# Optimization experiments

Hardware: AMD Instinct MI355X
Metric: run time of the kernel (lower is better)

The kernel has to match this reference:

```python
import jax, jax.numpy as jnp
import numpy as np
from jax import lax

B, N, D, L, EDGE_H, NGNN = 8, 128, 256, 64, 64, 3


def setup_inputs() -> dict:
    key = jax.random.key(0)
    ks = iter(jax.random.split(key, 64))
    def nrm(shape, s=0.02):
        return jax.random.normal(next(ks), shape, jnp.float32) * s
    inp = {}
    inp["node_feats"] = jax.random.uniform(next(ks), (B, N, 11), jnp.float32)
    inp["edge_feats"] = jax.random.normal(next(ks), (B, N, N, 3), jnp.float32)
    inp["adj_mask"] = jax.random.randint(next(ks), (B, N, N), 0, 2).astype(bool)
    inp["layer_costs"] = jax.random.uniform(next(ks), (B, L), jnp.float32)
    inp["global_dynamic"] = jax.random.uniform(next(ks), (B, 2), jnp.float32)
    inp["p_node_w"] = nrm((11, D)); inp["p_node_b"] = jnp.zeros((D,), jnp.float32)
    inp["g_w1"] = nrm((NGNN, D + 3, EDGE_H)); inp["g_b1"] = jnp.zeros((NGNN, EDGE_H), jnp.float32)
    inp["g_w2"] = nrm((NGNN, EDGE_H, D)); inp["g_b2"] = jnp.zeros((NGNN, D), jnp.float32)
    inp["u_w1"] = nrm((NGNN, 3 * D, D)); inp["u_b1"] = jnp.zeros((NGNN, D), jnp.float32)
    inp["u_w2"] = nrm((NGNN, D, D)); inp["u_b2"] = jnp.zeros((NGNN, D), jnp.float32)
    inp["ln_g"] = jnp.ones((NGNN, D), jnp.float32); inp["ln_b"] = jnp.zeros((NGNN, D), jnp.float32)
    inp["conv_w"] = nrm((32, 1, 4)); inp["conv_b"] = jnp.zeros((32,), jnp.float32)
    inp["lp_w"] = nrm((32 * 31, D)); inp["lp_b"] = jnp.zeros((D,), jnp.float32)
    inp["q_w"] = nrm((2 * D + 2, D)); inp["q_b"] = jnp.zeros((D,), jnp.float32)
    inp["k_w"] = nrm((D, D)); inp["k_b"] = jnp.zeros((D,), jnp.float32)
    inp["s_w1"] = nrm((D + 2, D)); inp["s_b1"] = jnp.zeros((D,), jnp.float32)
    inp["s_w2"] = nrm((D, 1)); inp["s_b2"] = jnp.zeros((1,), jnp.float32)
    inp["v_w1"] = nrm((2 * D + 2, D)); inp["v_b1"] = jnp.zeros((D,), jnp.float32)
    inp["v_w2"] = nrm((D, 1)); inp["v_b2"] = jnp.zeros((1,), jnp.float32)
    return inp


def _ecgc(h, edge_feats, adj_bool, gw1, gb1, gw2, gb2, uw1, ub1, uw2, ub2, lng, lnb):
    Bh, Nn, Dd = h.shape
    # h_j: features of sender node j broadcast over receiver axis -> (B, N, N, D)
    h_j = jnp.broadcast_to(h[:, None, :, :], (Bh, Nn, Nn, Dd))
    gate_in = jnp.concatenate([h_j, edge_feats], axis=-1)            # (B,N,N,D+3)
    gates = jax.nn.sigmoid(jax.nn.relu(gate_in @ gw1 + gb1) @ gw2 + gb2)
    msg = gates * h_j                                                # (B,N,N,D)
    m = adj_bool.astype(h.dtype)[..., None]
    cnt = jnp.maximum(m.sum(axis=2), 1.0)                            # (B,N,1)
    agg_mean = (msg * m).sum(axis=2) / cnt                           # (B,N,D)
    agg_max = jnp.where(adj_bool[..., None], msg, -jnp.inf).max(axis=2)
    agg_max = jnp.where(jnp.isinf(agg_max), 0.0, agg_max)
    ui = jnp.concatenate([h, agg_mean, agg_max], axis=-1)            # (B,N,3D)
    x = h + (jax.nn.relu(ui @ uw1 + ub1) @ uw2 + ub2)
    mu = x.mean(-1, keepdims=True)
    var = ((x - mu) ** 2).mean(-1, keepdims=True)
    return (x - mu) * lax.rsqrt(var + 1e-5) * lng + lnb


def reference(node_feats, edge_feats, adj_mask, layer_costs, global_dynamic,
              p_node_w, p_node_b, g_w1, g_b1, g_w2, g_b2, u_w1, u_b1, u_w2, u_b2,
              ln_g, ln_b, conv_w, conv_b, lp_w, lp_b, q_w, q_b, k_w, k_b,
              s_w1, s_b1, s_w2, s_b2, v_w1, v_b1, v_w2, v_b2):
    # layer cost encoder: Conv1d(1,32,k=4,s=2) + ReLU, flatten, Linear
    le = lax.conv_general_dilated(layer_costs[:, None, :], conv_w, (2,), 'VALID',
                                  dimension_numbers=('NCH', 'OIH', 'NCH'))
    le = jax.nn.relu(le + conv_b[None, :, None])                     # (B,32,31)
    layer_embed = le.reshape(le.shape[0], -1) @ lp_w + lp_b          # (B,D)
    h = node_feats @ p_node_w + p_node_b                             # (B,N,D)
    for i in range(g_w1.shape[0]):
        h = _ecgc(h, edge_feats, adj_mask, g_w1[i], g_b1[i], g_w2[i], g_b2[i],
                  u_w1[i], u_b1[i], u_w2[i], u_b2[i], ln_g[i], ln_b[i])
    w = (node_feats[:, :, 0] * node_feats[:, :, 7])[..., None]       # (B,N,1)
    graph_embed = (w * h).sum(axis=1) / jnp.maximum(w.sum(axis=1), 1e-8)
    qi = jnp.concatenate([graph_embed, layer_embed, global_dynamic], axis=-1)
    query = qi @ q_w + q_b                                           # (B,D)
    keys = h @ k_w + k_b                                             # (B,N,D)
    device_scores = jnp.einsum('bnd,bd->bn', keys, query) / jnp.sqrt(jnp.float32(query.shape[-1]))
    si = jnp.concatenate([graph_embed, global_dynamic], axis=-1)
    stop_logit = jax.nn.relu(si @ s_w1 + s_b1) @ s_w2 + s_b2         # (B,1)
    all_logits = jnp.concatenate([device_scores, stop_logit], axis=1)
    value = jax.nn.relu(qi @ v_w1 + v_b1) @ v_w2 + v_b2              # (B,1)
    return all_logits, value, h
```

## Files before the change

kernel.cpp:

```cpp
#include <hip/hip_runtime.h>
#include <hip/hip_bf16.h>
#include <math.h>

#define BB 8
#define NN_ 128
#define DD 256
#define LL 64
#define EH 64
#define NG 3

typedef __attribute__((ext_vector_type(8))) short bs8;
typedef __attribute__((ext_vector_type(4))) float f4;

__device__ __forceinline__ short f2bf(float f) {
    __hip_bfloat16 h = __float2bfloat16(f);
    return *reinterpret_cast<short*>(&h);
}

__device__ __forceinline__ float blockReduceSum(float v, float* sRed) {
    int tid = threadIdx.x;
    __syncthreads();
    sRed[tid] = v;
    __syncthreads();
    for (int s = 128; s > 0; s >>= 1) {
        if (tid < s) sRed[tid] += sRed[tid + s];
        __syncthreads();
    }
    return sRed[0];
}

__global__ __launch_bounds__(256) void k_detect(const unsigned char* __restrict__ adj,
                                                int* __restrict__ mode) {
    __shared__ int sOff, sBig;
    const int tid = threadIdx.x;
    if (tid == 0) { sOff = 0; sBig = 0; }
    __syncthreads();
    int off = 0, big = 0;
    #pragma unroll
    for (int k = 0; k < 4; ++k) {
        unsigned char v = adj[tid * 4 + k];
        if (v > 1) big = 1;
        if (k != 0 && v != 0) off = 1;
    }
    if (off) atomicOr(&sOff, 1);
    if (big) atomicOr(&sBig, 1);
    __syncthreads();
    if (tid == 0) mode[0] = sBig ? 2 : (sOff ? 0 : 1);
}

__global__ __launch_bounds__(256) void k_prep(
    const float* __restrict__ uw1, const float* __restrict__ uw2,
    unsigned short* __restrict__ w1t, unsigned short* __restrict__ w2t)
{
    const int blk = blockIdx.x, tid = threadIdx.x;
    const float* src; unsigned short* dst; int K, kt, dt;
    if (blk < 144) {
        int l = blk / 48, t = blk % 48; kt = t >> 2; dt = t & 3;
        src = uw1 + (size_t)l * 768 * 256; dst = w1t + (size_t)l * 256 * 768; K = 768;
    } else {
        int x = blk - 144; int l = x / 16, t = x % 16; kt = t >> 2; dt = t & 3;
        src = uw2 + (size_t)l * 65536; dst = w2t + (size_t)l * 65536; K = 256;
    }
    __shared__ float sT[64][65];
    #pragma unroll
    for (int q = 0; q < 16; ++q) {
        int idx = q * 256 + tid;
        int kk = idx >> 6, dd = idx & 63;
        sT[kk][dd] = src[(size_t)(kt * 64 + kk) * 256 + dt * 64 + dd];
    }
    __syncthreads();
    const int d = tid >> 2, kc = (tid & 3) * 16;
    unsigned short* drow = dst + (size_t)(dt * 64 + d) * K + kt * 64 + kc;
    #pragma unroll
    for (int i = 0; i < 16; ++i) drow[i] = (unsigned short)f2bf(sT[kc + i][d]);
}

__global__ __launch_bounds__(256) void k_prepg(
    const float* __restrict__ gw2, unsigned short* __restrict__ g2t)
{
    const int blk = blockIdx.x, tid = threadIdx.x;
    const int l = blk >> 2, dt = blk & 3;
    const float* src = gw2 + (size_t)l * 64 * 256;
    unsigned short* dst = g2t + (size_t)l * 256 * 64;
    __shared__ float sT[64][65];
    #pragma unroll
    for (int q = 0; q < 16; ++q) {
        int idx = q * 256 + tid;
        int kk = idx >> 6, dd = idx & 63;
        sT[kk][dd] = src[(size_t)kk * 256 + dt * 64 + dd];
    }
    __syncthreads();
    const int d = tid >> 2, kc = (tid & 3) * 16;
    unsigned short* drow = dst + (size_t)(dt * 64 + d) * 64 + kc;
    #pragma unroll
    for (int i = 0; i < 16; ++i) drow[i] = (unsigned short)f2bf(sT[kc + i][d]);
}

__global__ __launch_bounds__(256) void k_nodeproj(
    const float* __restrict__ nf, const float* __restrict__ w,
    const float* __restrict__ bias, float* __restrict__ h)
{
    const int row = blockIdx.x, tid = threadIdx.x;
    __shared__ float sF[11];
    if (tid < 11) sF[tid] = nf[(size_t)row * 11 + tid];
    __syncthreads();
    float a = bias[tid];
    #pragma unroll
    for (int f = 0; f < 11; ++f) a += sF[f] * w[f * DD + tid];
    h[(size_t)row * DD + tid] = a;
}

__global__ __launch_bounds__(256) void k_conv(
    const float* __restrict__ lc, const float* __restrict__ cw,
    const float* __restrict__ cb, float* __restrict__ conv)
{
    const int b = blockIdx.x, tid = threadIdx.x;
    __shared__ float sC[LL];
    if (tid < LL) sC[tid] = lc[b * LL + tid];
    __syncthreads();
    for (int idx = tid; idx < 992; idx += 256) {
        int c = idx / 31, t = idx % 31;
        float a = cb[c];
        #pragma unroll
        for (int k = 0; k < 4; ++k) a += sC[2 * t + k] * cw[c * 4 + k];
        conv[b * 992 + idx] = fmaxf(a, 0.f);
    }
}

__global__ __launch_bounds__(256) void k_lmm(
    const float* __restrict__ conv, const float* __restrict__ lpw,
    float* __restrict__ part)
{
    const int blk = blockIdx.x;
    const int b = blk >> 5, kseg = (blk >> 2) & 7, c4 = blk & 3;
    const int tid = threadIdx.x;
    const int d = tid & 63, ss = tid >> 6;
    __shared__ float sV[124];
    __shared__ float sP[4][64];
    if (tid < 124) sV[tid] = conv[b * 992 + kseg * 124 + tid];
    __syncthreads();
    float acc = 0.f;
    for (int k = ss; k < 124; k += 4)
        acc += sV[k] * lpw[(size_t)(kseg * 124 + k) * DD + c4 * 64 + d];
    sP[ss][d] = acc;
    __syncthreads();
    if (ss == 0)
        part[(b * 32 + kseg * 4 + c4) * 64 + d] = sP[0][d] + sP[1][d] + sP[2][d] + sP[3][d];
}

__global__ __launch_bounds__(256) void k_lred(
    const float* __restrict__ part, const float* __restrict__ lpb,
    float* __restrict__ le)
{
    const int b = blockIdx.x, tid = threadIdx.x;
    const int c4 = tid >> 6, d = tid & 63;
    float a = lpb[tid];
    #pragma unroll
    for (int kseg = 0; kseg < 8; ++kseg)
        a += part[(b * 32 + kseg * 4 + c4) * 64 + d];
    le[b * DD + tid] = a;
}

__global__ __launch_bounds__(256) void k_pregate(
    const float* __restrict__ h, const float* __restrict__ gw1,
    const float* __restrict__ gb1, float* __restrict__ preg)
{
    const int tid = threadIdx.x;
    const int row0 = blockIdx.x * 4;
    const int r = tid >> 6, t = tid & 63;
    __shared__ float sH[4][DD];
    for (int idx = tid; idx < 4 * DD; idx += 256)
        sH[idx >> 8][idx & 255] = h[(size_t)row0 * DD + idx];
    __syncthreads();
    float a = gb1[t];
    for (int k = 0; k < DD; ++k) a += sH[r][k] * gw1[k * EH + t];
    preg[(size_t)(row0 + r) * EH + t] = a;
}

template<int PRE>
__global__ __launch_bounds__(256) void k_edge(
    const float* __restrict__ h, const float* __restrict__ preg,
    const float* __restrict__ edge, const void* __restrict__ adj,
    const int* __restrict__ mode,
    const float* __restrict__ gw1,
    const float* __restrict__ gw2,
    const unsigned short* __restrict__ g2t,
    const float* __restrict__ gb2,
    float* __restrict__ agg_mean, float* __restrict__ agg_max)
{
    const int tid = threadIdx.x;
    const int bi = blockIdx.x;
    const int b = bi >> 7;
    const int lane = tid & 63, w = tid >> 6;
    const int lrow = lane >> 4, lcol = lane & 15;
    const int md = mode[0];

    __shared__ __align__(16) unsigned int sHid[4096];
    __shared__ __align__(16) unsigned short sB[PRE ? 16 : 16384];
    __shared__ float sWe[192];
    __shared__ float sE[384];
    __shared__ unsigned long long sMask[2];

    if (tid < 192) sWe[tid] = gw1[16384 + tid];
    const float* eB = edge + (size_t)bi * 384;
    for (int idx = tid; idx < 384; idx += 256) sE[idx] = eB[idx];
    if (tid < 128) {
        int mv;
        if (md == 1)      mv = ((const int*)adj)[(size_t)bi * NN_ + tid] != 0;
        else if (md == 2) mv = ((const float*)adj)[(size_t)bi * NN_ + tid] != 0.f;
        else              mv = ((const unsigned char*)adj)[(size_t)bi * NN_ + tid] != 0;
        unsigned long long bal = __ballot(mv);
        if ((tid & 63) == 0) sMask[tid >> 6] = bal;
    }
    __syncthreads();

    const float* pB = preg + (size_t)b * NN_ * EH;
    #pragma unroll
    for (int q = 0; q < 16; ++q) {
        int idx = q * 256 + tid;
        int j = idx >> 5, p = idx & 31;
        float2 pv = *(const float2*)(pB + j * EH + 2 * p);
        float e0 = sE[j * 3], e1 = sE[j * 3 + 1], e2 = sE[j * 3 + 2];
        int t0 = 2 * p, t1 = t0 + 1;
        float v0 = fmaxf(pv.x + e0 * sWe[t0] + e1 * sWe[64 + t0] + e2 * sWe[128 + t0], 0.f);
        float v1 = fmaxf(pv.y + e0 * sWe[t1] + e1 * sWe[64 + t1] + e2 * sWe[128 + t1], 0.f);
        unsigned int pk = (unsigned int)(unsigned short)f2bf(v0) |
                          ((unsigned int)(unsigned short)f2bf(v1) << 16);
        sHid[j * 32 + (p ^ ((j & 7) << 2))] = pk;
    }
    if constexpr (!PRE) {
        #pragma unroll
        for (int q = 0; q < 64; ++q) {
            int idx = q * 256 + tid;
            int k = idx >> 8, d = idx & 255;
            sB[(d * 64 + k) ^ ((d & 7) << 3)] = (unsigned short)f2bf(gw2[idx]);
        }
    }
    __syncthreads();

    const unsigned long long m0 = sMask[0], m1 = sMask[1];
    const float cntf = (float)(__popcll(m0) + __popcll(m1));

    bs8 bfr[4][2];
    float bg[4];
    #pragma unroll
    for (int nt = 0; nt < 4; ++nt) {
        int d = w * 64 + nt * 16 + lcol;
        bg[nt] = gb2[d];
        #pragma unroll
        for (int ks = 0; ks < 2; ++ks) {
            int k0 = ks * 32 + lrow * 8;
            if constexpr (PRE)
                bfr[nt][ks] = *(const bs8*)(g2t + (size_t)d * 64 + k0);
            else
                bfr[nt][ks] = *(const bs8*)(sB + ((d * 64 + k0) ^ ((d & 7) << 3)));
        }
    }

    const float* hB = h + (size_t)b * NN_ * DD;
    float vs[4] = {0.f, 0.f, 0.f, 0.f};
    float vm[4] = {-INFINITY, -INFINITY, -INFINITY, -INFINITY};

    #pragma unroll
    for (int pp = 0; pp < 2; ++pp) {
        f4 acc[4][4] = {};
        #pragma unroll
        for (int ks = 0; ks < 2; ++ks) {
            bs8 afr[4];
            #pragma unroll
            for (int m = 0; m < 4; ++m) {
                int j = pp * 64 + m * 16 + lcol;
                int k0 = ks * 32 + lrow * 8;
                afr[m] = *(const bs8*)(sHid + (j * 32 + ((k0 >> 1) ^ ((j & 7) << 2))));
            }
            #pragma unroll
            for (int m = 0; m < 4; ++m)
                #pragma unroll
                for (int nt = 0; nt < 4; ++nt)
                    acc[m][nt] = __builtin_amdgcn_mfma_f32_16x16x32_bf16(
                        afr[m], bfr[nt][ks], acc[m][nt], 0, 0, 0);
        }
        const unsigned long long mw = pp ? m1 : m0;
        #pragma unroll
        for (int m = 0; m < 4; ++m) {
            #pragma unroll
            for (int nt = 0; nt < 4; ++nt) {
                int dnt = w * 64 + nt * 16 + lcol;
                #pragma unroll
                for (int r = 0; r < 4; ++r) {
                    int bit = m * 16 + lrow * 4 + r;
                    float x = acc[m][nt][r] + bg[nt];
                    float g = __builtin_amdgcn_rcpf(1.0f + __expf(-x));
                    float msg = g * hB[(pp * 64 + bit) * DD + dnt];
                    int on = (int)((mw >> bit) & 1ULL);
                    vs[nt] += on ? msg : 0.f;
                    vm[nt] = fmaxf(vm[nt], on ? msg : -INFINITY);
                }
            }
        }
    }

    #pragma unroll
    for (int nt = 0; nt < 4; ++nt) {
        float s = vs[nt];
        s += __shfl_xor(s, 16); s += __shfl_xor(s, 32);
        vs[nt] = s;
        float m = vm[nt];
        m = fmaxf(m, __shfl_xor(m, 16)); m = fmaxf(m, __shfl_xor(m, 32));
        vm[nt] = m;
    }
    const int g = lrow;
    float ssel = (g == 0) ? vs[0] : (g == 1) ? vs[1] : (g == 2) ? vs[2] : vs[3];
    float msel = (g == 0) ? vm[0] : (g == 1) ? vm[1] : (g == 2) ? vm[2] : vm[3];
    const int d = w * 64 + lane;
    agg_mean[(size_t)bi * DD + d] = ssel / fmaxf(cntf, 1.f);
    agg_max[(size_t)bi * DD + d] = (cntf > 0.f) ? msel : 0.f;
}

__global__ __launch_bounds__(256) void k_upd(
    const float* __restrict__ h, const float* __restrict__ amean,
    const float* __restrict__ amax,
    const unsigned short* __restrict__ w1t,
    const float* __restrict__ ub1,
    const unsigned short* __restrict__ w2t,
    const float* __restrict__ ub2,
    const float* __restrict__ lng, const float* __restrict__ lnb,
    float* __restrict__ hout, float* __restrict__ out2)
{
    const int tid = threadIdx.x;
    const int row0 = blockIdx.x * 4;
    const int lane = tid & 63, w = tid >> 6;
    const int lcol = lane & 15, lrow = lane >> 4;

    __shared__ __align__(16) unsigned int sX32[16 * 384];
    __shared__ __align__(16) unsigned short sH16[16 * 256];
    __shared__ float sRes[4][256];
    __shared__ float sOut[4][256];

    {
        const int j = w;
        const float* hR = h + (size_t)(row0 + j) * DD;
        const float* mR = amean + (size_t)(row0 + j) * DD;
        const float* xR = amax + (size_t)(row0 + j) * DD;
        #pragma unroll
        for (int q = 0; q < 6; ++q) {
            int p = lane + q * 64;
            int k = 2 * p;
            float2 v;
            if (k < 256)      { v = *(const float2*)(hR + k); sRes[j][k] = v.x; sRes[j][k + 1] = v.y; }
            else if (k < 512)   v = *(const float2*)(mR + (k - 256));
            else                v = *(const float2*)(xR + (k - 512));
            unsigned int pk = (unsigned int)(unsigned short)f2bf(v.x) |
                              ((unsigned int)(unsigned short)f2bf(v.y) << 16);
            sX32[j * 384 + (p ^ (j << 2))] = pk;
        }
    }
    __syncthreads();

    const char* sXb = (const char*)sX32;
    const unsigned short* w1r = w1t + (size_t)(w * 64 + lcol) * 768;
    f4 a0 = {0.f, 0.f, 0.f, 0.f}, a1 = a0, a2 = a0, a3 = a0;
    #pragma unroll 4
    for (int ks = 0; ks < 24; ++ks) {
        int k0 = ks * 32 + lrow * 8;
        bs8 av = *(const bs8*)(sXb + lcol * 1536 + ((((k0 >> 3) ^ (lcol & 7))) << 4));
        bs8 b0 = *(const bs8*)(w1r + k0);
        bs8 b1 = *(const bs8*)(w1r + 16 * 768 + k0);
        bs8 b2 = *(const bs8*)(w1r + 32 * 768 + k0);
        bs8 b3 = *(const bs8*)(w1r + 48 * 768 + k0);
        a0 = __builtin_amdgcn_mfma_f32_16x16x32_bf16(av, b0, a0, 0, 0, 0);
        a1 = __builtin_amdgcn_mfma_f32_16x16x32_bf16(av, b1, a1, 0, 0, 0);
        a2 = __builtin_amdgcn_mfma_f32_16x16x32_bf16(av, b2, a2, 0, 0, 0);
        a3 = __builtin_amdgcn_mfma_f32_16x16x32_bf16(av, b3, a3, 0, 0, 0);
    }
    if (lrow == 0) {
        #pragma unroll
        for (int nt = 0; nt < 4; ++nt) {
            int d = w * 64 + nt * 16 + lcol;
            float bb = ub1[d];
            f4 A = (nt == 0) ? a0 : (nt == 1) ? a1 : (nt == 2) ? a2 : a3;
            #pragma unroll
            for (int r = 0; r < 4; ++r) {
                float hv = fmaxf(A[r] + bb, 0.f);
                sH16[r * 256 + (d ^ (r << 3))] = (unsigned short)f2bf(hv);
            }
        }
    }
    __syncthreads();

    const unsigned short* w2r = w2t + (size_t)(w * 64 + lcol) * 256;
    f4 c0 = {0.f, 0.f, 0.f, 0.f}, c1 = c0, c2 = c0, c3 = c0;
    #pragma unroll
    for (int ks = 0; ks < 8; ++ks) {
        int k0 = ks * 32 + lrow * 8;
        bs8 av = *(const bs8*)((const char*)sH16 + lcol * 512 + ((((k0 >> 3) ^ (lcol & 7))) << 4));
        bs8 b0 = *(const bs8*)(w2r + k0);
        bs8 b1 = *(const bs8*)(w2r + 16 * 256 + k0);
        bs8 b2 = *(const bs8*)(w2r + 32 * 256 + k0);
        bs8 b3 = *(const bs8*)(w2r + 48 * 256 + k0);
        c0 = __builtin_amdgcn_mfma_f32_16x16x32_bf16(av, b0, c0, 0, 0, 0);
        c1 = __builtin_amdgcn_mfma_f32_16x16x32_bf16(av, b1, c1, 0, 0, 0);
        c2 = __builtin_amdgcn_mfma_f32_16x16x32_bf16(av, b2, c2, 0, 0, 0);
        c3 = __builtin_amdgcn_mfma_f32_16x16x32_bf16(av, b3, c3, 0, 0, 0);
    }
    if (lrow == 0) {
        #pragma unroll
        for (int nt = 0; nt < 4; ++nt) {
            int d = w * 64 + nt * 16 + lcol;
            float bb = ub2[d];
            f4 C = (nt == 0) ? c0 : (nt == 1) ? c1 : (nt == 2) ? c2 : c3;
            #pragma unroll
            for (int r = 0; r < 4; ++r)
                sOut[r][d] = C[r] + bb + sRes[r][d];
        }
    }
    __syncthreads();

    float xv[4], s = 0.f;
    #pragma unroll
    for (int q = 0; q < 4; ++q) { xv[q] = sOut[w][lane + 64 * q]; s += xv[q]; }
    #pragma unroll
    for (int off = 1; off < 64; off <<= 1) s += __shfl_xor(s, off);
    const float mu = s * (1.f / DD);
    float s2 = 0.f;
    #pragma unroll
    for (int q = 0; q < 4; ++q) { float d = xv[q] - mu; s2 += d * d; }
    #pragma unroll
    for (int off = 1; off < 64; off <<= 1) s2 += __shfl_xor(s2, off);
    const float inv = rsqrtf(s2 * (1.f / DD) + 1e-5f);
    #pragma unroll
    for (int q = 0; q < 4; ++q) {
        int c = lane + 64 * q;
        float res = (xv[q] - mu) * inv * lng[c] + lnb[c];
        hout[(size_t)(row0 + w) * DD + c] = res;
        if (out2) out2[(size_t)(row0 + w) * DD + c] = res;
    }
}

__global__ __launch_bounds__(256) void k_update(
    const float* __restrict__ agg_mean, const float* __restrict__ agg_max,
    const float* __restrict__ uw1, const float* __restrict__ ub1,
    const float* __restrict__ uw2, const float* __restrict__ ub2,
    const float* __restrict__ lng, const float* __restrict__ lnb,
    float* __restrict__ h, float* __restrict__ out2)
{
    const int tid = threadIdx.x;
    const int row0 = blockIdx.x * 4;
    __shared__ float sUi[4][3 * DD];
    __shared__ float sHid[4][DD];
    __shared__ float sRed[256];
    for (int idx = tid; idx < 4 * 3 * DD; idx += 256) {
        int r = idx / (3 * DD), k = idx % (3 * DD);
        int row = row0 + r;
        float v;
        if (k < DD)            v = h[(size_t)row * DD + k];
        else if (k < 2 * DD)   v = agg_mean[(size_t)row * DD + (k - DD)];
        else                   v = agg_max[(size_t)row * DD + (k - 2 * DD)];
        sUi[r][k] = v;
    }
    __syncthreads();
    float b1 = ub1[tid];
    float a0 = b1, a1 = b1, a2 = b1, a3 = b1;
    for (int k = 0; k < 3 * DD; ++k) {
        float wv = uw1[k * DD + tid];
        a0 += sUi[0][k] * wv; a1 += sUi[1][k] * wv;
        a2 += sUi[2][k] * wv; a3 += sUi[3][k] * wv;
    }
    sHid[0][tid] = fmaxf(a0, 0.f); sHid[1][tid] = fmaxf(a1, 0.f);
    sHid[2][tid] = fmaxf(a2, 0.f); sHid[3][tid] = fmaxf(a3, 0.f);
    __syncthreads();
    float b2 = ub2[tid];
    float x[4] = {b2, b2, b2, b2};
    for (int k = 0; k < DD; ++k) {
        float wv = uw2[k * DD + tid];
        x[0] += sHid[0][k] * wv; x[1] += sHid[1][k] * wv;
        x[2] += sHid[2][k] * wv; x[3] += sHid[3][k] * wv;
    }
    #pragma unroll
    for (int r = 0; r < 4; ++r) x[r] += h[(size_t)(row0 + r) * DD + tid];
    const float g = lng[tid], be = lnb[tid];
    for (int r = 0; r < 4; ++r) {
        float mu = blockReduceSum(x[r], sRed) * (1.f / DD);
        float dc = x[r] - mu;
        float var = blockReduceSum(dc * dc, sRed) * (1.f / DD);
        float res = dc * rsqrtf(var + 1e-5f) * g + be;
        h[(size_t)(row0 + r) * DD + tid] = res;
        if (out2) out2[(size_t)(row0 + r) * DD + tid] = res;
    }
}

__global__ __launch_bounds__(256) void k_gembed(
    const float* __restrict__ nf, const float* __restrict__ h, float* __restrict__ ge)
{
    const int b = blockIdx.x, tid = threadIdx.x;
    __shared__ float sW[NN_];
    __shared__ float sRed[256];
    if (tid < NN_) {
        const float* p = nf + ((size_t)b * NN_ + tid) * 11;
        sW[tid] = p[0] * p[7];
    }
    __syncthreads();
    float part = (tid < NN_) ? sW[tid] : 0.f;
    float wsum = blockReduceSum(part, sRed);
    float acc = 0.f;
    for (int n = 0; n < NN_; ++n) acc += sW[n] * h[((size_t)b * NN_ + n) * DD + tid];
    ge[b * DD + tid] = acc / fmaxf(wsum, 1e-8f);
}

__global__ __launch_bounds__(256) void k_hmm(
    const float* __restrict__ ge, const float* __restrict__ le,
    const float* __restrict__ gd,
    const float* __restrict__ qw, const float* __restrict__ sw1,
    const float* __restrict__ vw1, float* __restrict__ part)
{
    const int blk = blockIdx.x;
    const int m = blk >> 5, kseg = (blk >> 2) & 7, c4 = blk & 3;
    const int tid = threadIdx.x;
    const int d = tid & 63, ks = tid >> 6;
    const int K = (m == 1) ? 258 : 514;
    const int kc = (m == 1) ? 33 : 65;
    const int k0 = kseg * kc;
    const int klen = min(k0 + kc, K) - k0;
    __shared__ float sX[8 * 66];
    __shared__ float sP[4][8][64];
    for (int idx = tid; idx < 8 * kc; idx += 256) {
        int b = idx / kc, kk = idx % kc, k = k0 + kk;
        float v = 0.f;
        if (k < K) {
            if (m == 1) v = (k < 256) ? ge[b * DD + k] : gd[b * 2 + (k - 256)];
            else        v = (k < 256) ? ge[b * DD + k]
                          : (k < 512) ? le[b * DD + (k - 256)]
                                      : gd[b * 2 + (k - 512)];
        }
        sX[b * 66 + kk] = v;
    }
    __syncthreads();
    const float* W = (m == 0) ? qw : (m == 1) ? sw1 : vw1;
    const int dg = c4 * 64 + d;
    float acc[8] = {0.f, 0.f, 0.f, 0.f, 0.f, 0.f, 0.f, 0.f};
    for (int kk = ks; kk < klen; kk += 4) {
        float wv = W[(size_t)(k0 + kk) * DD + dg];
        #pragma unroll
        for (int b = 0; b < 8; ++b) acc[b] += sX[b * 66 + kk] * wv;
    }
    #pragma unroll
    for (int b = 0; b < 8; ++b) sP[ks][b][d] = acc[b];
    __syncthreads();
    for (int idx = tid; idx < 8 * 64; idx += 256) {
        int b = idx >> 6, dd = idx & 63;
        float sum = sP[0][b][dd] + sP[1][b][dd] + sP[2][b][dd] + sP[3][b][dd];
        part[((m * 8 + kseg) * 8 + b) * DD + c4 * 64 + dd] = sum;
    }
}

__global__ __launch_bounds__(256) void k_hfin(
    const float* __restrict__ part,
    const float* __restrict__ qb, const float* __restrict__ sb1,
    const float* __restrict__ vb1,
    const float* __restrict__ sw2, const float* __restrict__ sb2,
    const float* __restrict__ vw2, const float* __restrict__ vb2,
    float* __restrict__ query, float* __restrict__ out)
{
    const int b = blockIdx.x, tid = threadIdx.x;
    __shared__ float sRed[256];
    float q = qb[tid], s = sb1[tid], v = vb1[tid];
    #pragma unroll
    for (int kseg = 0; kseg < 8; ++kseg) {
        q += part[((0 * 8 + kseg) * 8 + b) * DD + tid];
        s += part[((1 * 8 + kseg) * 8 + b) * DD + tid];
        v += part[((2 * 8 + kseg) * 8 + b) * DD + tid];
    }
    query[b * DD + tid] = q;
    s = fmaxf(s, 0.f); v = fmaxf(v, 0.f);
    float stop = blockReduceSum(s * sw2[tid], sRed);
    float val  = blockReduceSum(v * vw2[tid], sRed);
    if (tid == 0) {
        out[b * 129 + 128] = stop + sb2[0];
        out[1032 + b] = val + vb2[0];
    }
}

__global__ __launch_bounds__(256) void k_scores(
    const float* __restrict__ h, const float* __restrict__ kw,
    const float* __restrict__ kb, const float* __restrict__ query,
    float* __restrict__ out)
{
    const int tid = threadIdx.x;
    const int row0 = blockIdx.x * 4;
    __shared__ float sH[4][DD];
    __shared__ float sRed[256];
    for (int idx = tid; idx < 4 * DD; idx += 256)
        sH[idx >> 8][idx & 255] = h[(size_t)row0 * DD + idx];
    __syncthreads();
    float bb = kb[tid];
    float a0 = bb, a1 = bb, a2 = bb, a3 = bb;
    for (int k = 0; k < DD; ++k) {
        float wv = kw[k * DD + tid];
        a0 += sH[0][k] * wv; a1 += sH[1][k] * wv;
        a2 += sH[2][k] * wv; a3 += sH[3][k] * wv;
    }
    const int b = row0 >> 7;
    const float q = query[b * DD + tid];
    float s0 = blockReduceSum(a0 * q, sRed);
    float s1 = blockReduceSum(a1 * q, sRed);
    float s2 = blockReduceSum(a2 * q, sRed);
    float s3 = blockReduceSum(a3 * q, sRed);
    if (tid == 0) {
        int n0 = row0 & (NN_ - 1);
        out[b * 129 + n0 + 0] = s0 * 0.0625f;
        out[b * 129 + n0 + 1] = s1 * 0.0625f;
        out[b * 129 + n0 + 2] = s2 * 0.0625f;
        out[b * 129 + n0 + 3] = s3 * 0.0625f;
    }
}

extern "C" void kernel_launch(void* const* d_in, const int* in_sizes, int n_in,
                              void* d_out, int out_size, void* d_ws, size_t ws_size,
                              hipStream_t stream) {
    (void)in_sizes; (void)n_in; (void)out_size;
    const float* nf  = (const float*)d_in[0];
    const float* ef  = (const float*)d_in[1];
    const void*  adj = d_in[2];
    const float* lc  = (const float*)d_in[3];
    const float* gd  = (const float*)d_in[4];
    const float* pnw = (const float*)d_in[5];
    const float* pnb = (const float*)d_in[6];
    const float* gw1 = (const float*)d_in[7];
    const float* gb1 = (const float*)d_in[8];
    const float* gw2 = (const float*)d_in[9];
    const float* gb2 = (const float*)d_in[10];
    const float* uw1 = (const float*)d_in[11];
    const float* ub1 = (const float*)d_in[12];
    const float* uw2 = (const float*)d_in[13];
    const float* ub2 = (const float*)d_in[14];
    const float* lng = (const float*)d_in[15];
    const float* lnb = (const float*)d_in[16];
    const float* cw  = (const float*)d_in[17];
    const float* cb  = (const float*)d_in[18];
    const float* lpw = (const float*)d_in[19];
    const float* lpb = (const float*)d_in[20];
    const float* qw  = (const float*)d_in[21];
    const float* qb  = (const float*)d_in[22];
    const float* kw  = (const float*)d_in[23];
    const float* kb  = (const float*)d_in[24];
    const float* sw1 = (const float*)d_in[25];
    const float* sb1 = (const float*)d_in[26];
    const float* sw2 = (const float*)d_in[27];
    const float* sb2 = (const float*)d_in[28];
    const float* vw1 = (const float*)d_in[29];
    const float* vb1 = (const float*)d_in[30];
    const float* vw2 = (const float*)d_in[31];
    const float* vb2 = (const float*)d_in[32];

    float* ws = (float*)d_ws;
    float* h     = ws;
    float* preg  = ws + 262144;
    float* amean = ws + 327680;
    float* amax  = ws + 589824;
    float* le    = ws + 851968;
    float* ge    = ws + 854016;
    float* query = ws + 856064;
    int*   mode  = (int*)(ws + 862208);
    unsigned short* uw1t = (unsigned short*)(ws + 862212);
    unsigned short* uw2t = (unsigned short*)(ws + 1157124);
    unsigned short* g2t  = (unsigned short*)(ws + 1255428);
    const size_t NEED = (size_t)1280004 * 4;
    const bool pre = ws_size >= NEED;
    float* conv  = amax;
    float* lpart = amean;
    float* hpart = amean;
    float* out   = (float*)d_out;

    k_detect<<<1, 256, 0, stream>>>((const unsigned char*)adj, mode);
    if (pre) {
        k_prep<<<192, 256, 0, stream>>>(uw1, uw2, uw1t, uw2t);
        k_prepg<<<12, 256, 0, stream>>>(gw2, g2t);
    }
    k_nodeproj<<<BB * NN_, 256, 0, stream>>>(nf, pnw, pnb, h);
    k_conv<<<BB, 256, 0, stream>>>(lc, cw, cb, conv);
    k_lmm<<<256, 256, 0, stream>>>(conv, lpw, lpart);
    k_lred<<<BB, 256, 0, stream>>>(lpart, lpb, le);
    for (int i = 0; i < NG; ++i) {
        const float* gw1i = gw1 + (size_t)i * 259 * EH;
        float* out2sel = (i == NG - 1) ? (out + 1040) : (float*)nullptr;
        k_pregate<<<BB * NN_ / 4, 256, 0, stream>>>(h, gw1i, gb1 + i * EH, preg);
        if (pre) {
            k_edge<1><<<BB * NN_, 256, 0, stream>>>(h, preg, ef, adj, mode, gw1i,
                                                    gw2 + (size_t)i * EH * DD,
                                                    g2t + (size_t)i * 16384,
                                                    gb2 + i * DD, amean, amax);
            k_upd<<<BB * NN_ / 4, 256, 0, stream>>>(h, amean, amax,
                                                    uw1t + (size_t)i * 196608, ub1 + i * DD,
                                                    uw2t + (size_t)i * 65536, ub2 + i * DD,
                                                    lng + i * DD, lnb + i * DD, h, out2sel);
        } else {
            k_edge<0><<<BB * NN_, 256, 0, stream>>>(h, preg, ef, adj, mode, gw1i,
                                                    gw2 + (size_t)i * EH * DD,
                                                    (const unsigned short*)nullptr,
                                                    gb2 + i * DD, amean, amax);
            k_update<<<BB * NN_ / 4, 256, 0, stream>>>(amean, amax,
                                                       uw1 + (size_t)i * 3 * DD * DD, ub1 + i * DD,
                                                       uw2 + (size_t)i * DD * DD, ub2 + i * DD,
                                                       lng + i * DD, lnb + i * DD, h, out2sel);
        }
    }
    k_gembed<<<BB, 256, 0, stream>>>(nf, h, ge);
    k_hmm<<<96, 256, 0, stream>>>(ge, le, gd, qw, sw1, vw1, hpart);
    k_hfin<<<BB, 256, 0, stream>>>(hpart, qb, sb1, vb1, sw2, sb2, vw2, vb2, query, out);
    k_scores<<<BB * NN_ / 4, 256, 0, stream>>>(h, kw, kb, query, out);
}
```

Measured before the change: 216.4 us.

## Merge prep kernels, fuse conv/lred, and use bf16 MFMA for pregate and scores

Folds adjacency-mode detection and all weight transposes into a single prep launch, fuses the conv step into the layer matmul, and moves the layer-embed reduction into the head kernel, which removes several small launches. The pregate and key-score matmuls switch from scalar fp32 loops to bf16 MFMA over pre-transposed weights. The fp32 fallback path for small workspaces is dropped, and gembed gets four independent accumulators. This lowers precision in two more matmuls and now assumes the workspace is always large enough.

```diff
diff --git a/kernel.cpp b/kernel.cpp
--- a/kernel.cpp
+++ b/kernel.cpp
@@ -17,6 +17,13 @@
     return *reinterpret_cast<short*>(&h);
 }
 
+__device__ __forceinline__ bs8 cvt8(const float* __restrict__ p) {
+    bs8 r;
+    #pragma unroll
+    for (int i = 0; i < 8; ++i) r[i] = f2bf(p[i]);
+    return r;
+}
+
 __device__ __forceinline__ float blockReduceSum(float v, float* sRed) {
     int tid = threadIdx.x;
     __syncthreads();
@@ -29,69 +36,52 @@
     return sRed[0];
 }
 
-__global__ __launch_bounds__(256) void k_detect(const unsigned char* __restrict__ adj,
-                                                int* __restrict__ mode) {
-    __shared__ int sOff, sBig;
-    const int tid = threadIdx.x;
-    if (tid == 0) { sOff = 0; sBig = 0; }
-    __syncthreads();
-    int off = 0, big = 0;
-    #pragma unroll
-    for (int k = 0; k < 4; ++k) {
-        unsigned char v = adj[tid * 4 + k];
-        if (v > 1) big = 1;
-        if (k != 0 && v != 0) off = 1;
-    }
-    if (off) atomicOr(&sOff, 1);
-    if (big) atomicOr(&sBig, 1);
-    __syncthreads();
-    if (tid == 0) mode[0] = sBig ? 2 : (sOff ? 0 : 1);
-}
-
 __global__ __launch_bounds__(256) void k_prep(
     const float* __restrict__ uw1, const float* __restrict__ uw2,
-    unsigned short* __restrict__ w1t, unsigned short* __restrict__ w2t)
+    const float* __restrict__ gw2, const float* __restrict__ gw1,
+    const float* __restrict__ kw, const unsigned char* __restrict__ adj,
+    unsigned short* __restrict__ w1t, unsigned short* __restrict__ w2t,
+    unsigned short* __restrict__ g2t, unsigned short* __restrict__ g1t,
+    unsigned short* __restrict__ kwt, int* __restrict__ mode)
 {
     const int blk = blockIdx.x, tid = threadIdx.x;
-    const float* src; unsigned short* dst; int K, kt, dt;
-    if (blk < 144) {
-        int l = blk / 48, t = blk % 48; kt = t >> 2; dt = t & 3;
-        src = uw1 + (size_t)l * 768 * 256; dst = w1t + (size_t)l * 256 * 768; K = 768;
-    } else {
-        int x = blk - 144; int l = x / 16, t = x % 16; kt = t >> 2; dt = t & 3;
-        src = uw2 + (size_t)l * 65536; dst = w2t + (size_t)l * 65536; K = 256;
-    }
+    if (blk == 232) {
+        __shared__ int sOff, sBig;
+        if (tid == 0) { sOff = 0; sBig = 0; }
+        __syncthreads();
+        int off = 0, big = 0;
+        #pragma unroll
+        for (int k = 0; k < 4; ++k) {
+            unsigned char v = adj[tid * 4 + k];
+            if (v > 1) big = 1;
+            if (k != 0 && v != 0) off = 1;
+        }
+        if (off) atomicOr(&sOff, 1);
+        if (big) atomicOr(&sBig, 1);
+        __syncthreads();
+        if (tid == 0) mode[0] = sBig ? 2 : (sOff ? 0 : 1);
+        return;
+    }
+    const float* src; unsigned short* dst; int K, kt, dt, srcw = 256;
+    if (blk < 144)      { int l = blk / 48, t = blk % 48; kt = t >> 2; dt = t & 3;
+                          src = uw1 + (size_t)l * 196608; dst = w1t + (size_t)l * 196608; K = 768; }
+    else if (blk < 192) { int x = blk - 144, l = x / 16, t = x % 16; kt = t >> 2; dt = t & 3;
+                          src = uw2 + (size_t)l * 65536; dst = w2t + (size_t)l * 65536; K = 256; }
+    else if (blk < 204) { int x = blk - 192, l = x >> 2; kt = 0; dt = x & 3;
+                          src = gw2 + (size_t)l * 16384; dst = g2t + (size_t)l * 16384; K = 64; }
+    else if (blk < 216) { int x = blk - 204, l = x >> 2; kt = x & 3; dt = 0; srcw = 64;
+                          src = gw1 + (size_t)l * 16576; dst = g1t + (size_t)l * 16384; K = 256; }
+    else                { int x = blk - 216; kt = x >> 2; dt = x & 3;
+                          src = kw; dst = kwt; K = 256; }
     __shared__ float sT[64][65];
     #pragma unroll
     for (int q = 0; q < 16; ++q) {
-        int idx = q * 256 + tid;
-        int kk = idx >> 6, dd = idx & 63;
-        sT[kk][dd] = src[(size_t)(kt * 64 + kk) * 256 + dt * 64 + dd];
+        int idx = q * 256 + tid, kk = idx >> 6, dd = idx & 63;
+        sT[kk][dd] = src[(size_t)(kt * 64 + kk) * srcw + dt * 64 + dd];
     }
     __syncthreads();
     const int d = tid >> 2, kc = (tid & 3) * 16;
     unsigned short* drow = dst + (size_t)(dt * 64 + d) * K + kt * 64 + kc;
-    #pragma unroll
-    for (int i = 0; i < 16; ++i) drow[i] = (unsigned short)f2bf(sT[kc + i][d]);
-}
-
-__global__ __launch_bounds__(256) void k_prepg(
-    const float* __restrict__ gw2, unsigned short* __restrict__ g2t)
-{
-    const int blk = blockIdx.x, tid = threadIdx.x;
-    const int l = blk >> 2, dt = blk & 3;
-    const float* src = gw2 + (size_t)l * 64 * 256;
-    unsigned short* dst = g2t + (size_t)l * 256 * 64;
-    __shared__ float sT[64][65];
-    #pragma unroll
-    for (int q = 0; q < 16; ++q) {
-        int idx = q * 256 + tid;
-        int kk = idx >> 6, dd = idx & 63;
-        sT[kk][dd] = src[(size_t)kk * 256 + dt * 64 + dd];
-    }
-    __syncthreads();
-    const int d = tid >> 2, kc = (tid & 3) * 16;
-    unsigned short* drow = dst + (size_t)(dt * 64 + d) * 64 + kc;
     #pragma unroll
     for (int i = 0; i < 16; ++i) drow[i] = (unsigned short)f2bf(sT[kc + i][d]);
 }
@@ -110,34 +100,28 @@
     h[(size_t)row * DD + tid] = a;
 }
 
-__global__ __launch_bounds__(256) void k_conv(
+__global__ __launch_bounds__(256) void k_lmm(
     const float* __restrict__ lc, const float* __restrict__ cw,
-    const float* __restrict__ cb, float* __restrict__ conv)
-{
-    const int b = blockIdx.x, tid = threadIdx.x;
-    __shared__ float sC[LL];
-    if (tid < LL) sC[tid] = lc[b * LL + tid];
-    __syncthreads();
-    for (int idx = tid; idx < 992; idx += 256) {
-        int c = idx / 31, t = idx % 31;
-        float a = cb[c];
-        #pragma unroll
-        for (int k = 0; k < 4; ++k) a += sC[2 * t + k] * cw[c * 4 + k];
-        conv[b * 992 + idx] = fmaxf(a, 0.f);
-    }
-}
-
-__global__ __launch_bounds__(256) void k_lmm(
-    const float* __restrict__ conv, const float* __restrict__ lpw,
+    const float* __restrict__ cb, const float* __restrict__ lpw,
     float* __restrict__ part)
 {
     const int blk = blockIdx.x;
     const int b = blk >> 5, kseg = (blk >> 2) & 7, c4 = blk & 3;
     const int tid = threadIdx.x;
     const int d = tid & 63, ss = tid >> 6;
+    __shared__ float sC[LL];
     __shared__ float sV[124];
     __shared__ float sP[4][64];
-    if (tid < 124) sV[tid] = conv[b * 992 + kseg * 124 + tid];
+    if (tid < LL) sC[tid] = lc[b * LL + tid];
+    __syncthreads();
+    if (tid < 124) {
+        int idx = kseg * 124 + tid;
+        int c = idx / 31, t = idx - c * 31;
+        float a = cb[c];
+        #pragma unroll
+        for (int k = 0; k < 4; ++k) a += sC[2 * t + k] * cw[c * 4 + k];
+        sV[tid] = fmaxf(a, 0.f);
+    }
     __syncthreads();
     float acc = 0.f;
     for (int k = ss; k < 124; k += 4)
@@ -148,42 +132,35 @@
         part[(b * 32 + kseg * 4 + c4) * 64 + d] = sP[0][d] + sP[1][d] + sP[2][d] + sP[3][d];
 }
 
-__global__ __launch_bounds__(256) void k_lred(
-    const float* __restrict__ part, const float* __restrict__ lpb,
-    float* __restrict__ le)
-{
-    const int b = blockIdx.x, tid = threadIdx.x;
-    const int c4 = tid >> 6, d = tid & 63;
-    float a = lpb[tid];
-    #pragma unroll
-    for (int kseg = 0; kseg < 8; ++kseg)
-        a += part[(b * 32 + kseg * 4 + c4) * 64 + d];
-    le[b * DD + tid] = a;
-}
-
 __global__ __launch_bounds__(256) void k_pregate(
-    const float* __restrict__ h, const float* __restrict__ gw1,
+    const float* __restrict__ h, const unsigned short* __restrict__ g1t,
     const float* __restrict__ gb1, float* __restrict__ preg)
 {
-    const int tid = threadIdx.x;
-    const int row0 = blockIdx.x * 4;
-    const int r = tid >> 6, t = tid & 63;
-    __shared__ float sH[4][DD];
-    for (int idx = tid; idx < 4 * DD; idx += 256)
-        sH[idx >> 8][idx & 255] = h[(size_t)row0 * DD + idx];
-    __syncthreads();
-    float a = gb1[t];
-    for (int k = 0; k < DD; ++k) a += sH[r][k] * gw1[k * EH + t];
-    preg[(size_t)(row0 + r) * EH + t] = a;
-}
-
-template<int PRE>
+    const int tid = threadIdx.x, blk = blockIdx.x;
+    const int row0 = blk * 16;
+    const int lane = tid & 63, w = tid >> 6;
+    const int lcol = lane & 15, lrow = lane >> 4;
+    const float* aR = h + (size_t)(row0 + lcol) * DD;
+    const unsigned short* bR = g1t + (size_t)(w * 16 + lcol) * 256;
+    f4 acc = {0.f, 0.f, 0.f, 0.f};
+    #pragma unroll
+    for (int ks = 0; ks < 8; ++ks) {
+        int k0 = ks * 32 + lrow * 8;
+        bs8 av = cvt8(aR + k0);
+        bs8 bv = *(const bs8*)(bR + k0);
+        acc = __builtin_amdgcn_mfma_f32_16x16x32_bf16(av, bv, acc, 0, 0, 0);
+    }
+    const float gb = gb1[w * 16 + lcol];
+    #pragma unroll
+    for (int r = 0; r < 4; ++r)
+        preg[(size_t)(row0 + lrow * 4 + r) * EH + w * 16 + lcol] = acc[r] + gb;
+}
+
 __global__ __launch_bounds__(256) void k_edge(
     const float* __restrict__ h, const float* __restrict__ preg,
     const float* __restrict__ edge, const void* __restrict__ adj,
     const int* __restrict__ mode,
     const float* __restrict__ gw1,
-    const float* __restrict__ gw2,
     const unsigned short* __restrict__ g2t,
     const float* __restrict__ gb2,
     float* __restrict__ agg_mean, float* __restrict__ agg_max)
@@ -196,7 +173,6 @@
     const int md = mode[0];
 
     __shared__ __align__(16) unsigned int sHid[4096];
-    __shared__ __align__(16) unsigned short sB[PRE ? 16 : 16384];
     __shared__ float sWe[192];
     __shared__ float sE[384];
     __shared__ unsigned long long sMask[2];
@@ -228,14 +204,6 @@
                           ((unsigned int)(unsigned short)f2bf(v1) << 16);
         sHid[j * 32 + (p ^ ((j & 7) << 2))] = pk;
     }
-    if constexpr (!PRE) {
-        #pragma unroll
-        for (int q = 0; q < 64; ++q) {
-            int idx = q * 256 + tid;
-            int k = idx >> 8, d = idx & 255;
-            sB[(d * 64 + k) ^ ((d & 7) << 3)] = (unsigned short)f2bf(gw2[idx]);
-        }
-    }
     __syncthreads();
 
     const unsigned long long m0 = sMask[0], m1 = sMask[1];
@@ -250,10 +218,7 @@
         #pragma unroll
         for (int ks = 0; ks < 2; ++ks) {
             int k0 = ks * 32 + lrow * 8;
-            if constexpr (PRE)
-                bfr[nt][ks] = *(const bs8*)(g2t + (size_t)d * 64 + k0);
-            else
-                bfr[nt][ks] = *(const bs8*)(sB + ((d * 64 + k0) ^ ((d & 7) << 3)));
+            bfr[nt][ks] = *(const bs8*)(g2t + (size_t)d * 64 + k0);
         }
     }
 
@@ -437,58 +402,6 @@
     }
 }
 
-__global__ __launch_bounds__(256) void k_update(
-    const float* __restrict__ agg_mean, const float* __restrict__ agg_max,
-    const float* __restrict__ uw1, const float* __restrict__ ub1,
-    const float* __restrict__ uw2, const float* __restrict__ ub2,
-    const float* __restrict__ lng, const float* __restrict__ lnb,
-    float* __restrict__ h, float* __restrict__ out2)
-{
-    const int tid = threadIdx.x;
-    const int row0 = blockIdx.x * 4;
-    __shared__ float sUi[4][3 * DD];
-    __shared__ float sHid[4][DD];
-    __shared__ float sRed[256];
-    for (int idx = tid; idx < 4 * 3 * DD; idx += 256) {
-        int r = idx / (3 * DD), k = idx % (3 * DD);
-        int row = row0 + r;
-        float v;
-        if (k < DD)            v = h[(size_t)row * DD + k];
-        else if (k < 2 * DD)   v = agg_mean[(size_t)row * DD + (k - DD)];
-        else                   v = agg_max[(size_t)row * DD + (k - 2 * DD)];
-        sUi[r][k] = v;
-    }
-    __syncthreads();
-    float b1 = ub1[tid];
-    float a0 = b1, a1 = b1, a2 = b1, a3 = b1;
-    for (int k = 0; k < 3 * DD; ++k) {
-        float wv = uw1[k * DD + tid];
-        a0 += sUi[0][k] * wv; a1 += sUi[1][k] * wv;
-        a2 += sUi[2][k] * wv; a3 += sUi[3][k] * wv;
-    }
-    sHid[0][tid] = fmaxf(a0, 0.f); sHid[1][tid] = fmaxf(a1, 0.f);
-    sHid[2][tid] = fmaxf(a2, 0.f); sHid[3][tid] = fmaxf(a3, 0.f);
-    __syncthreads();
-    float b2 = ub2[tid];
-    float x[4] = {b2, b2, b2, b2};
-    for (int k = 0; k < DD; ++k) {
-        float wv = uw2[k * DD + tid];
-        x[0] += sHid[0][k] * wv; x[1] += sHid[1][k] * wv;
-        x[2] += sHid[2][k] * wv; x[3] += sHid[3][k] * wv;
-    }
-    #pragma unroll
-    for (int r = 0; r < 4; ++r) x[r] += h[(size_t)(row0 + r) * DD + tid];
-    const float g = lng[tid], be = lnb[tid];
-    for (int r = 0; r < 4; ++r) {
-        float mu = blockReduceSum(x[r], sRed) * (1.f / DD);
-        float dc = x[r] - mu;
-        float var = blockReduceSum(dc * dc, sRed) * (1.f / DD);
-        float res = dc * rsqrtf(var + 1e-5f) * g + be;
-        h[(size_t)(row0 + r) * DD + tid] = res;
-        if (out2) out2[(size_t)(row0 + r) * DD + tid] = res;
-    }
-}
-
 __global__ __launch_bounds__(256) void k_gembed(
     const float* __restrict__ nf, const float* __restrict__ h, float* __restrict__ ge)
 {
@@ -502,16 +415,23 @@
     __syncthreads();
     float part = (tid < NN_) ? sW[tid] : 0.f;
     float wsum = blockReduceSum(part, sRed);
-    float acc = 0.f;
-    for (int n = 0; n < NN_; ++n) acc += sW[n] * h[((size_t)b * NN_ + n) * DD + tid];
-    ge[b * DD + tid] = acc / fmaxf(wsum, 1e-8f);
+    const float* hb = h + (size_t)b * NN_ * DD + tid;
+    float a0 = 0.f, a1 = 0.f, a2 = 0.f, a3 = 0.f;
+    for (int n = 0; n < 32; ++n) {
+        a0 += sW[n]      * hb[(size_t)n * DD];
+        a1 += sW[n + 32] * hb[(size_t)(n + 32) * DD];
+        a2 += sW[n + 64] * hb[(size_t)(n + 64) * DD];
+        a3 += sW[n + 96] * hb[(size_t)(n + 96) * DD];
+    }
+    ge[b * DD + tid] = (a0 + a1 + a2 + a3) / fmaxf(wsum, 1e-8f);
 }
 
 __global__ __launch_bounds__(256) void k_hmm(
-    const float* __restrict__ ge, const float* __restrict__ le,
-    const float* __restrict__ gd,
+    const float* __restrict__ ge, const float* __restrict__ gd,
     const float* __restrict__ qw, const float* __restrict__ sw1,
-    const float* __restrict__ vw1, float* __restrict__ part)
+    const float* __restrict__ vw1,
+    const float* __restrict__ lpb, const float* __restrict__ lpart,
+    float* __restrict__ part)
 {
     const int blk = blockIdx.x;
     const int m = blk >> 5, kseg = (blk >> 2) & 7, c4 = blk & 3;
@@ -524,15 +444,20 @@
     __shared__ float sX[8 * 66];
     __shared__ float sP[4][8][64];
     for (int idx = tid; idx < 8 * kc; idx += 256) {
-        int b = idx / kc, kk = idx % kc, k = k0 + kk;
+        int bb = idx / kc, kk = idx % kc, k = k0 + kk;
         float v = 0.f;
         if (k < K) {
-            if (m == 1) v = (k < 256) ? ge[b * DD + k] : gd[b * 2 + (k - 256)];
-            else        v = (k < 256) ? ge[b * DD + k]
-                          : (k < 512) ? le[b * DD + (k - 256)]
-                                      : gd[b * 2 + (k - 512)];
-        }
-        sX[b * 66 + kk] = v;
+            if (m == 1) v = (k < 256) ? ge[bb * DD + k] : gd[bb * 2 + (k - 256)];
+            else if (k < 256) v = ge[bb * DD + k];
+            else if (k < 512) {
+                int e = k - 256;
+                v = lpb[e];
+                #pragma unroll
+                for (int s = 0; s < 8; ++s)
+                    v += lpart[(bb * 32 + s * 4 + (e >> 6)) * 64 + (e & 63)];
+            } else v = gd[bb * 2 + (k - 512)];
+        }
+        sX[bb * 66 + kk] = v;
     }
     __syncthreads();
     const float* W = (m == 0) ? qw : (m == 1) ? sw1 : vw1;
@@ -541,15 +466,15 @@
     for (int kk = ks; kk < klen; kk += 4) {
         float wv = W[(size_t)(k0 + kk) * DD + dg];
         #pragma unroll
-        for (int b = 0; b < 8; ++b) acc[b] += sX[b * 66 + kk] * wv;
-    }
-    #pragma unroll
-    for (int b = 0; b < 8; ++b) sP[ks][b][d] = acc[b];
+        for (int bb = 0; bb < 8; ++bb) acc[bb] += sX[bb * 66 + kk] * wv;
+    }
+    #pragma unroll
+    for (int bb = 0; bb < 8; ++bb) sP[ks][bb][d] = acc[bb];
     __syncthreads();
     for (int idx = tid; idx < 8 * 64; idx += 256) {
-        int b = idx >> 6, dd = idx & 63;
-        float sum = sP[0][b][dd] + sP[1][b][dd] + sP[2][b][dd] + sP[3][b][dd];
-        part[((m * 8 + kseg) * 8 + b) * DD + c4 * 64 + dd] = sum;
+        int bb = idx >> 6, dd = idx & 63;
+        float sum = sP[0][bb][dd] + sP[1][bb][dd] + sP[2][bb][dd] + sP[3][bb][dd];
+        part[((m * 8 + kseg) * 8 + bb) * DD + c4 * 64 + dd] = sum;
     }
 }
 
@@ -581,43 +506,57 @@
 }
 
 __global__ __launch_bounds__(256) void k_scores(
-    const float* __restrict__ h, const float* __restrict__ kw,
+    const float* __restrict__ h, const unsigned short* __restrict__ kwt,
     const float* __restrict__ kb, const float* __restrict__ query,
     float* __restrict__ out)
 {
-    const int tid = threadIdx.x;
-    const int row0 = blockIdx.x * 4;
-    __shared__ float sH[4][DD];
-    __shared__ float sRed[256];
-    for (int idx = tid; idx < 4 * DD; idx += 256)
-        sH[idx >> 8][idx & 255] = h[(size_t)row0 * DD + idx];
-    __syncthreads();
-    float bb = kb[tid];
-    float a0 = bb, a1 = bb, a2 = bb, a3 = bb;
-    for (int k = 0; k < DD; ++k) {
-        float wv = kw[k * DD + tid];
-        a0 += sH[0][k] * wv; a1 += sH[1][k] * wv;
-        a2 += sH[2][k] * wv; a3 += sH[3][k] * wv;
-    }
-    const int b = row0 >> 7;
-    const float q = query[b * DD + tid];
-    float s0 = blockReduceSum(a0 * q, sRed);
-    float s1 = blockReduceSum(a1 * q, sRed);
-    float s2 = blockReduceSum(a2 * q, sRed);
-    float s3 = blockReduceSum(a3 * q, sRed);
-    if (tid == 0) {
-        int n0 = row0 & (NN_ - 1);
-        out[b * 129 + n0 + 0] = s0 * 0.0625f;
-        out[b * 129 + n0 + 1] = s1 * 0.0625f;
-        out[b * 129 + n0 + 2] = s2 * 0.0625f;
-        out[b * 129 + n0 + 3] = s3 * 0.0625f;
+    const int tid = threadIdx.x, blk = blockIdx.x;
+    const int row0 = blk * 16, b = blk >> 3;
+    const int lane = tid & 63, w = tid >> 6;
+    const int lcol = lane & 15, lrow = lane >> 4;
+    __shared__ float sPart[4][16];
+    const float* aR = h + (size_t)(row0 + lcol) * DD;
+    f4 acc[4] = {};
+    #pragma unroll
+    for (int ks = 0; ks < 8; ++ks) {
+        int k0 = ks * 32 + lrow * 8;
+        bs8 av = cvt8(aR + k0);
+        #pragma unroll
+        for (int nt = 0; nt < 4; ++nt) {
+            bs8 bv = *(const bs8*)(kwt + (size_t)(w * 64 + nt * 16 + lcol) * 256 + k0);
+            acc[nt] = __builtin_amdgcn_mfma_f32_16x16x32_bf16(av, bv, acc[nt], 0, 0, 0);
+        }
+    }
+    float part[4] = {0.f, 0.f, 0.f, 0.f};
+    #pragma unroll
+    for (int nt = 0; nt < 4; ++nt) {
+        int col = w * 64 + nt * 16 + lcol;
+        float q = query[b * DD + col], kv = kb[col];
+        #pragma unroll
+        for (int r = 0; r < 4; ++r) part[r] += (acc[nt][r] + kv) * q;
+    }
+    #pragma unroll
+    for (int r = 0; r < 4; ++r) {
+        float s = part[r];
+        s += __shfl_xor(s, 1); s += __shfl_xor(s, 2);
+        s += __shfl_xor(s, 4); s += __shfl_xor(s, 8);
+        part[r] = s;
+    }
+    if (lcol == 0) {
+        #pragma unroll
+        for (int r = 0; r < 4; ++r) sPart[w][lrow * 4 + r] = part[r];
+    }
+    __syncthreads();
+    if (tid < 16) {
+        float s = sPart[0][tid] + sPart[1][tid] + sPart[2][tid] + sPart[3][tid];
+        out[b * 129 + (row0 & (NN_ - 1)) + tid] = s * 0.0625f;
     }
 }
 
 extern "C" void kernel_launch(void* const* d_in, const int* in_sizes, int n_in,
                               void* d_out, int out_size, void* d_ws, size_t ws_size,
                               hipStream_t stream) {
-    (void)in_sizes; (void)n_in; (void)out_size;
+    (void)in_sizes; (void)n_in; (void)out_size; (void)ws_size;
     const float* nf  = (const float*)d_in[0];
     const float* ef  = (const float*)d_in[1];
     const void*  adj = d_in[2];
@@ -657,55 +596,40 @@
     float* preg  = ws + 262144;
     float* amean = ws + 327680;
     float* amax  = ws + 589824;
-    float* le    = ws + 851968;
-    float* ge    = ws + 854016;
-    float* query = ws + 856064;
-    int*   mode  = (int*)(ws + 862208);
-    unsigned short* uw1t = (unsigned short*)(ws + 862212);
-    unsigned short* uw2t = (unsigned short*)(ws + 1157124);
-    unsigned short* g2t  = (unsigned short*)(ws + 1255428);
-    const size_t NEED = (size_t)1280004 * 4;
-    const bool pre = ws_size >= NEED;
-    float* conv  = amax;
-    float* lpart = amean;
-    float* hpart = amean;
+    float* ge    = ws + 851968;
+    float* query = ws + 854016;
+    float* lpart = ws + 856064;
+    float* hpart = ws + 872448;
+    int*   mode  = (int*)(ws + 921600);
+    unsigned short* uw1t = (unsigned short*)(ws + 921604);
+    unsigned short* uw2t = (unsigned short*)(ws + 1216516);
+    unsigned short* g2t  = (unsigned short*)(ws + 1314820);
+    unsigned short* g1t  = (unsigned short*)(ws + 1339396);
+    unsigned short* kwt  = (unsigned short*)(ws + 1363972);
     float* out   = (float*)d_out;
 
-    k_detect<<<1, 256, 0, stream>>>((const unsigned char*)adj, mode);
-    if (pre) {
-        k_prep<<<192, 256, 0, stream>>>(uw1, uw2, uw1t, uw2t);
-        k_prepg<<<12, 256, 0, stream>>>(gw2, g2t);
-    }
+    k_prep<<<233, 256, 0, stream>>>(uw1, uw2, gw2, gw1, kw,
+                                    (const unsigned char*)adj,
+                                    uw1t, uw2t, g2t, g1t, kwt, mode);
     k_nodeproj<<<BB * NN_, 256, 0, stream>>>(nf, pnw, pnb, h);
-    k_conv<<<BB, 256, 0, stream>>>(lc, cw, cb, conv);
-    k_lmm<<<256, 256, 0, stream>>>(conv, lpw, lpart);
-    k_lred<<<BB, 256, 0, stream>>>(lpart, lpb, le);
+    k_lmm<<<256, 256, 0, stream>>>(lc, cw, cb, lpw, lpart);
+    k_pregate<<<BB * NN_ / 16, 256, 0, stream>>>(h, g1t, gb1, preg);
     for (int i = 0; i < NG; ++i) {
         const float* gw1i = gw1 + (size_t)i * 259 * EH;
         float* out2sel = (i == NG - 1) ? (out + 1040) : (float*)nullptr;
-        k_pregate<<<BB * NN_ / 4, 256, 0, stream>>>(h, gw1i, gb1 + i * EH, preg);
-        if (pre) {
-            k_edge<1><<<BB * NN_, 256, 0, stream>>>(h, preg, ef, adj, mode, gw1i,
-                                                    gw2 + (size_t)i * EH * DD,
-                                                    g2t + (size_t)i * 16384,
-                                                    gb2 + i * DD, amean, amax);
-            k_upd<<<BB * NN_ / 4, 256, 0, stream>>>(h, amean, amax,
-                                                    uw1t + (size_t)i * 196608, ub1 + i * DD,
-                                                    uw2t + (size_t)i * 65536, ub2 + i * DD,
-                                                    lng + i * DD, lnb + i * DD, h, out2sel);
-        } else {
-            k_edge<0><<<BB * NN_, 256, 0, stream>>>(h, preg, ef, adj, mode, gw1i,
-                                                    gw2 + (size_t)i * EH * DD,
-                                                    (const unsigned short*)nullptr,
-                                                    gb2 + i * DD, amean, amax);
-            k_update<<<BB * NN_ / 4, 256, 0, stream>>>(amean, amax,
-                                                       uw1 + (size_t)i * 3 * DD * DD, ub1 + i * DD,
-                                                       uw2 + (size_t)i * DD * DD, ub2 + i * DD,
-                                                       lng + i * DD, lnb + i * DD, h, out2sel);
-        }
+        k_edge<<<BB * NN_, 256, 0, stream>>>(h, preg, ef, adj, mode, gw1i,
+                                             g2t + (size_t)i * 16384,
+                                             gb2 + i * DD, amean, amax);
+        k_upd<<<BB * NN_ / 4, 256, 0, stream>>>(h, amean, amax,
+                                                uw1t + (size_t)i * 196608, ub1 + i * DD,
+                                                uw2t + (size_t)i * 65536, ub2 + i * DD,
+                                                lng + i * DD, lnb + i * DD, h, out2sel);
+        if (i < NG - 1)
+            k_pregate<<<BB * NN_ / 16, 256, 0, stream>>>(h, g1t + (size_t)(i + 1) * 16384,
+                                                         gb1 + (i + 1) * EH, preg);
     }
     k_gembed<<<BB, 256, 0, stream>>>(nf, h, ge);
-    k_hmm<<<96, 256, 0, stream>>>(ge, le, gd, qw, sw1, vw1, hpart);
+    k_hmm<<<96, 256, 0, stream>>>(ge, gd, qw, sw1, vw1, lpb, lpart, hpart);
     k_hfin<<<BB, 256, 0, stream>>>(hpart, qb, sb1, vb1, sw2, sb2, vw2, vb2, query, out);
-    k_scores<<<BB * NN_ / 4, 256, 0, stream>>>(h, kw, kb, query, out);
-}
+    k_scores<<<BB * NN_ / 16, 256, 0, stream>>>(h, kwt, kb, query, out);
+}
```

Measured after the change: 198.8 us. -8.2%, faster.
